# Kernel tuning notes

Measured on AMD Instinct MI355X. Metric: run time of the kernel, lower is better.

## Reference

```python
import jax, jax.numpy as jnp
import numpy as np

N, E, B, STEPS, THETAS, F, R = 20000, 40000, 32, 32, 64, 3, 1.0


def setup_inputs() -> dict:
    key = jax.random.key(0)
    k1, k2, k3, k4 = jax.random.split(key, 4)
    x = jax.random.normal(k1, (N, F), dtype=jnp.float32)
    v = jax.random.normal(k2, (F, THETAS), dtype=jnp.float32)
    v = v / jnp.linalg.norm(v, axis=0, keepdims=True)  # sphere constraint on directions
    lin = jnp.linspace(-R, R, STEPS, dtype=jnp.float32)
    edge_index = jax.random.randint(k3, (2, E), 0, N, dtype=jnp.int64)
    batch = jnp.sort(jax.random.randint(k4, (N,), 0, B, dtype=jnp.int64))
    return {"x": x, "v": v, "lin": lin, "edge_index": edge_index, "batch": batch}


def _ecc(h, idx, lin, num_segments):
    # h: [M, T] heights; idx: [M] graph ids; lin: [S] thresholds
    # sigmoid(200*(lin - h)) -> [M, S, T], then segment-sum over M -> [B, S, T]
    e = jax.nn.sigmoid(200.0 * (lin[None, :, None] - h[:, None, :]))
    return jax.ops.segment_sum(e, idx, num_segments=num_segments)


def reference(x, v, lin, edge_index, batch):
    nh = x @ v                                            # [N, T] node heights
    eh = jnp.maximum(nh[edge_index[0]], nh[edge_index[1]])  # [E, T] edge heights (max of endpoints)
    edge_batch = batch[edge_index[0]]                     # [E]
    ect_nodes = _ecc(nh, batch, lin, B)                   # [B, S, T]
    ect_edges = _ecc(eh, edge_batch, lin, B)              # [B, S, T]
    return ect_nodes - ect_edges / 2
```

## Files before the change

kernel.cpp:

```cpp
#include <hip/hip_runtime.h>

#define N_NODES 20000
#define N_EDGES 40000
#define NB 32
#define NS 32
#define NT 64
#define NSC 160
#define NPREP 192
#define CAPB 1536
#define KBM 8
#define STEP200 12.9032258065f
#define WB 0.992f


__device__ __forceinline__ float bcast(float x, int j) {
    return __uint_as_float(__builtin_amdgcn_readlane(__float_as_uint(x), j));
}

__device__ __forceinline__ void accum_item(float h, float w, int lane,
                                           float* __restrict__ acc,
                                           float* __restrict__ fdiff) {
    const float t200h = 200.0f * h;
    const float u = (h + 1.0f) * 15.5f;
    const int kb = (int)ceilf(u - WB);
    const int ke = (int)floorf(u + WB) + 1;
#pragma unroll
    for (int j = 0; j < 2; j++) {
        const int s = kb + j;
        if (s < ke && s >= 0 && s < NS) {
            const float z = fmaf((float)s, STEP200, -200.0f) - t200h;
            const float sig = __builtin_amdgcn_rcpf(1.0f + __expf(-z));
            atomicAdd(&acc[s * NT + lane], w * sig);
        }
    }
    const int kec = min(max(ke, 0), NS);
    atomicAdd(&fdiff[kec * NT + lane], w);
}

__global__ __launch_bounds__(256) void prep_kernel(
        const float* __restrict__ x, const int* __restrict__ ei,
        const int* __restrict__ batch, int* __restrict__ ecnt,
        int* __restrict__ node_base, float4* __restrict__ sedge,
        float* __restrict__ out_zero) {
    const int t = threadIdx.x;
    const int bid = blockIdx.x;
    for (int idx = bid * 256 + t; idx < NB * NS * NT; idx += NPREP * 256)
        out_zero[idx] = 0.0f;

    if (bid < NSC) {
        __shared__ int h[NB];
        __shared__ int basep[NB];
        if (t < NB) h[t] = 0;
        __syncthreads();
        const int e = bid * 256 + t;
        int b = -1, s = 0, d = 0;
        if (e < N_EDGES) {
            s = ei[e];
            d = ei[N_EDGES + e];
            b = batch[s];
            atomicAdd(&h[b], 1);
        }
        __syncthreads();
        if (t < NB && h[t] > 0) {
            basep[t] = atomicAdd(&ecnt[t], h[t]);
            h[t] = 0;
        }
        __syncthreads();
        if (b >= 0) {
            const int p = atomicAdd(&h[b], 1);
            const int g = basep[b] + p;
            if (g < CAPB) {
                float4* ep = sedge + (size_t)(b * CAPB + g) * 2;
                ep[0] = make_float4(x[3 * s], x[3 * s + 1], x[3 * s + 2], x[3 * d]);
                ep[1] = make_float4(x[3 * d + 1], x[3 * d + 2], 0.0f, 0.0f);
            }
        }
    } else if (bid < NSC + 20) {
#pragma unroll
        for (int k = 0; k < 4; k++) {
            const int n = (bid - NSC) * 1024 + k * 256 + t;
            if (n < N_NODES) {
                const int bn = batch[n];
                const int bp = (n == 0) ? -1 : batch[n - 1];
                for (int q = bp + 1; q <= bn; q++) node_base[q] = n;
                if (n == N_NODES - 1)
                    for (int q = bn + 1; q <= NB; q++) node_base[q] = N_NODES;
            }
        }
    }
}

__global__ __launch_bounds__(256) void ect_main_kernel(
        const float* __restrict__ x, const float* __restrict__ v,
        const int* __restrict__ node_base, const int* __restrict__ ecnt,
        const float4* __restrict__ sedge, float* __restrict__ out) {
    __shared__ float acc[NS * NT];
    __shared__ float fdiff[(NS + 1) * NT];
    const int t = threadIdx.x;
#pragma unroll
    for (int j = 0; j < 8; j++) acc[t + 256 * j] = 0.0f;
    for (int idx = t; idx < (NS + 1) * NT; idx += 256) fdiff[idx] = 0.0f;
    __syncthreads();

    const int lane = t & 63;
    const int wid = __builtin_amdgcn_readfirstlane(t >> 6);
    const int b = blockIdx.x / KBM;
    const int slot = (blockIdx.x % KBM) * 4 + wid;
    const float v0 = v[lane], v1 = v[NT + lane], v2 = v[2 * NT + lane];

    const int nlo = node_base[b], nhi = node_base[b + 1];
    const int nn = nhi - nlo;
    const int ne = min(ecnt[b], CAPB);
    const int cn = (nn + 63) >> 6;
    const int ce = (ne + 63) >> 6;

    for (int c = slot; c < cn + ce; c += KBM * 4) {
        if (c < cn) {
            const int base = nlo + c * 64;
            const int cnt = min(nhi - base, 64);
            const int li = base + min(lane, cnt - 1);
            const float ax = x[3 * li], ay = x[3 * li + 1], az = x[3 * li + 2];
            for (int j = 0; j < cnt; j++) {
                const float h = fmaf(bcast(ax, j), v0,
                                fmaf(bcast(ay, j), v1, bcast(az, j) * v2));
                accum_item(h, 1.0f, lane, acc, fdiff);
            }
        } else {
            const int base = (c - cn) * 64;
            const int cnt = min(ne - base, 64);
            const int li = b * CAPB + base + min(lane, cnt - 1);
            const float4* ep = sedge + (size_t)li * 2;
            const float4 A = ep[0], Bv = ep[1];
            for (int j = 0; j < cnt; j++) {
                const float hs = fmaf(bcast(A.x, j), v0,
                                 fmaf(bcast(A.y, j), v1, bcast(A.z, j) * v2));
                const float hd = fmaf(bcast(A.w, j), v0,
                                 fmaf(bcast(Bv.x, j), v1, bcast(Bv.y, j) * v2));
                accum_item(fmaxf(hs, hd), -0.5f, lane, acc, fdiff);
            }
        }
    }
    __syncthreads();

    if (t < NT) {
        float run = 0.0f;
#pragma unroll
        for (int s = 0; s < NS; s++) {
            run += fdiff[s * NT + t];
            acc[s * NT + t] += run;
        }
    }
    __syncthreads();

    float* ob = out + b * (NS * NT);
#pragma unroll
    for (int j = 0; j < 8; j++) {
        const int idx = t + 256 * j;
        const float val = acc[idx];
        if (val != 0.0f) atomicAdd(&ob[idx], val);
    }
}

extern "C" void kernel_launch(void* const* d_in, const int* in_sizes, int n_in,
                              void* d_out, int out_size, void* d_ws, size_t ws_size,
                              hipStream_t stream) {
    const float* x   = (const float*)d_in[0];
    const float* v   = (const float*)d_in[1];
    const int*   ei  = (const int*)d_in[3];
    const int*   bat = (const int*)d_in[4];

    float* out = (float*)d_out;

    int* ecnt      = (int*)d_ws;
    int* node_base = ecnt + NB;
    float4* sedge  = (float4*)((int*)d_ws + 72);

    hipMemsetAsync(ecnt, 0, NB * sizeof(int), stream);
    prep_kernel<<<NPREP, 256, 0, stream>>>(x, ei, bat, ecnt, node_base, sedge, out);
    ect_main_kernel<<<NB * KBM, 256, 0, stream>>>(
        x, v, node_base, ecnt, sedge, out);
}
```

Before: 119.2 us.

## Replace global atomic output accumulation with per-block partials and reduce kernel

```diff
diff --git a/kernel.cpp b/kernel.cpp
--- a/kernel.cpp
+++ b/kernel.cpp
@@ -6,9 +6,11 @@
 #define NS 32
 #define NT 64
 #define NSC 160
-#define NPREP 192
+#define NPREP 180
 #define CAPB 1536
 #define KBM 8
+#define NBLKM (NB * KBM)
+#define SEG (NS * NT)
 #define STEP200 12.9032258065f
 #define WB 0.992f
 
@@ -40,12 +42,9 @@
 __global__ __launch_bounds__(256) void prep_kernel(
         const float* __restrict__ x, const int* __restrict__ ei,
         const int* __restrict__ batch, int* __restrict__ ecnt,
-        int* __restrict__ node_base, float4* __restrict__ sedge,
-        float* __restrict__ out_zero) {
+        int* __restrict__ node_base, float4* __restrict__ sedge) {
     const int t = threadIdx.x;
     const int bid = blockIdx.x;
-    for (int idx = bid * 256 + t; idx < NB * NS * NT; idx += NPREP * 256)
-        out_zero[idx] = 0.0f;
 
     if (bid < NSC) {
         __shared__ int h[NB];
@@ -75,7 +74,7 @@
                 ep[1] = make_float4(x[3 * d + 1], x[3 * d + 2], 0.0f, 0.0f);
             }
         }
-    } else if (bid < NSC + 20) {
+    } else {
 #pragma unroll
         for (int k = 0; k < 4; k++) {
             const int n = (bid - NSC) * 1024 + k * 256 + t;
@@ -93,8 +92,8 @@
 __global__ __launch_bounds__(256) void ect_main_kernel(
         const float* __restrict__ x, const float* __restrict__ v,
         const int* __restrict__ node_base, const int* __restrict__ ecnt,
-        const float4* __restrict__ sedge, float* __restrict__ out) {
-    __shared__ float acc[NS * NT];
+        const float4* __restrict__ sedge, float* __restrict__ part) {
+    __shared__ float acc[SEG];
     __shared__ float fdiff[(NS + 1) * NT];
     const int t = threadIdx.x;
 #pragma unroll
@@ -152,13 +151,25 @@
     }
     __syncthreads();
 
-    float* ob = out + b * (NS * NT);
+    const float4* a4 = (const float4*)acc;
+    float4* pb = (float4*)(part + (size_t)blockIdx.x * SEG);
 #pragma unroll
-    for (int j = 0; j < 8; j++) {
-        const int idx = t + 256 * j;
-        const float val = acc[idx];
-        if (val != 0.0f) atomicAdd(&ob[idx], val);
+    for (int j = 0; j < 2; j++) pb[t + 256 * j] = a4[t + 256 * j];
+}
+
+__global__ __launch_bounds__(256) void reduce_kernel(
+        const float* __restrict__ part, float* __restrict__ out) {
+    const int o4 = blockIdx.x * 256 + threadIdx.x;
+    const int b = o4 >> 9;
+    const int i4 = o4 & 511;
+    const float4* p = (const float4*)(part + (size_t)b * KBM * SEG) + i4;
+    float4 s = p[0];
+#pragma unroll
+    for (int k = 1; k < KBM; k++) {
+        const float4 q = p[k * (SEG / 4)];
+        s.x += q.x; s.y += q.y; s.z += q.z; s.w += q.w;
     }
+    ((float4*)out)[o4] = s;
 }
 
 extern "C" void kernel_launch(void* const* d_in, const int* in_sizes, int n_in,
@@ -174,9 +185,10 @@
     int* ecnt      = (int*)d_ws;
     int* node_base = ecnt + NB;
     float4* sedge  = (float4*)((int*)d_ws + 72);
+    float* part    = (float*)((int*)d_ws + 72 + NB * CAPB * 8);
 
     hipMemsetAsync(ecnt, 0, NB * sizeof(int), stream);
-    prep_kernel<<<NPREP, 256, 0, stream>>>(x, ei, bat, ecnt, node_base, sedge, out);
-    ect_main_kernel<<<NB * KBM, 256, 0, stream>>>(
-        x, v, node_base, ecnt, sedge, out);
+    prep_kernel<<<NPREP, 256, 0, stream>>>(x, ei, bat, ecnt, node_base, sedge);
+    ect_main_kernel<<<NBLKM, 256, 0, stream>>>(x, v, node_base, ecnt, sedge, part);
+    reduce_kernel<<<64, 256, 0, stream>>>(part, out);
 }
```

Result: no change. 121.4 us (+1.9%).
